# Kernel tuning notes

Measured on AMD Instinct MI355X. Metric: run time of the kernel, lower is better.

## Reference

```python
import jax, jax.numpy as jnp
import numpy as np

QLEN, KLEN, RLEN, BSZ, NHEAD, DHEAD = 512, 512, 1024, 8, 16, 64
SCALE = 0.125  # 1/sqrt(d_head)


def rel_shift(x, klen):
    # x: [q, r, b, n] -> [q, klen, b, n] (XLNet relative shift)
    q, r, b, n = x.shape
    x = x.reshape(r, q, b, n)[1:]
    x = x.reshape(q, r - 1, b, n)[:, :klen]
    return x


def setup_inputs() -> dict:
    key = jax.random.key(0)
    ks = jax.random.split(key, 9)
    q_head = jax.random.normal(ks[0], (QLEN, BSZ, NHEAD, DHEAD), jnp.float32)
    k_head_h = jax.random.normal(ks[1], (KLEN, BSZ, NHEAD, DHEAD), jnp.float32)
    v_head_h = jax.random.normal(ks[2], (KLEN, BSZ, NHEAD, DHEAD), jnp.float32)
    k_head_r = jax.random.normal(ks[3], (RLEN, BSZ, NHEAD, DHEAD), jnp.float32)
    seg_embed = jax.random.normal(ks[4], (2, NHEAD, DHEAD), jnp.float32)
    seg_mat = jax.random.randint(ks[5], (QLEN, KLEN, BSZ), 0, 2).astype(bool)
    r_w_bias = jax.random.normal(ks[6], (NHEAD, DHEAD), jnp.float32) * 0.02
    r_r_bias = jax.random.normal(ks[7], (NHEAD, DHEAD), jnp.float32) * 0.02
    r_s_bias = jax.random.normal(ks[8], (NHEAD, DHEAD), jnp.float32) * 0.02
    # causal attention mask: 1.0 where key position j > query position i
    attn_mask = (jnp.arange(KLEN)[None, :] > jnp.arange(QLEN)[:, None]).astype(jnp.float32)
    attn_mask = attn_mask[:, :, None, None]  # [q, k, 1, 1]
    return {
        "q_head": q_head, "k_head_h": k_head_h, "v_head_h": v_head_h,
        "k_head_r": k_head_r, "seg_embed": seg_embed, "seg_mat": seg_mat,
        "r_w_bias": r_w_bias, "r_r_bias": r_r_bias, "r_s_bias": r_s_bias,
        "attn_mask": attn_mask,
    }


def reference(q_head, k_head_h, v_head_h, k_head_r, seg_embed, seg_mat,
              r_w_bias, r_r_bias, r_s_bias, attn_mask):
    klen = k_head_h.shape[0]
    # content-based score: [q, k, b, n]
    ac = jnp.einsum('ibnd,jbnd->ijbn', q_head + r_w_bias, k_head_h)
    # position-based score with relative shift
    bd = jnp.einsum('ibnd,jbnd->ijbn', q_head + r_r_bias, k_head_r)
    bd = rel_shift(bd, klen)
    # segment-based score: ef [q, 2, b, n] -> select per (q,k,b) via seg_mat
    ef = jnp.einsum('ibnd,snd->isbn', q_head + r_s_bias, seg_embed)
    ef = jnp.where(seg_mat[:, :, :, None], ef[:, 1:, :, :], ef[:, :1, :, :])
    attn_score = (ac + bd + ef) * SCALE
    attn_score = attn_score - 1e30 * attn_mask
    attn_prob = jax.nn.softmax(attn_score, axis=1)  # softmax over key dim j
    # dropout is identity in eval mode
    attn_vec = jnp.einsum('ijbn,jbnd->ibnd', attn_prob, v_head_h)
    return attn_vec
```

## Files before the change

kernel.cpp:

```cpp
#include <hip/hip_runtime.h>

#define QLEN 512
#define KLEN 512
#define RLEN 1024
#define BSZ 8
#define NHEAD 16
#define DHEAD 64
#define SROW 8192
#define SCALEF 0.125f

typedef __bf16 bf16x8 __attribute__((ext_vector_type(8)));
typedef __bf16 bf16x4 __attribute__((ext_vector_type(4)));
typedef float  f32x4  __attribute__((ext_vector_type(4)));

__device__ __forceinline__ f32x4 mfma_bf16(bf16x8 a, bf16x8 b, f32x4 c) {
    return __builtin_amdgcn_mfma_f32_16x16x32_bf16(a, b, c, 0, 0, 0);
}

__device__ __forceinline__ bf16x8 cvt_frag(f32x4 a, f32x4 b) {
    bf16x8 f;
    f[0] = (__bf16)a[0]; f[1] = (__bf16)a[1]; f[2] = (__bf16)a[2]; f[3] = (__bf16)a[3];
    f[4] = (__bf16)b[0]; f[5] = (__bf16)b[1]; f[6] = (__bf16)b[2]; f[7] = (__bf16)b[3];
    return f;
}


__global__ void __launch_bounds__(256)
cvt_kernel(const float* __restrict__ src, __bf16* __restrict__ dst, int n4) {
    int idx = blockIdx.x * blockDim.x + threadIdx.x;
    const int stride = gridDim.x * blockDim.x;
    for (; idx < n4; idx += stride) {
        f32x4 v = ((const f32x4*)src)[idx];
        bf16x4 o;
        o[0] = (__bf16)v[0]; o[1] = (__bf16)v[1]; o[2] = (__bf16)v[2]; o[3] = (__bf16)v[3];
        ((bf16x4*)dst)[idx] = o;
    }
}

__global__ void __launch_bounds__(256)
vtr_kernel(const float* __restrict__ vh, __bf16* __restrict__ vt) {
    const int blk = blockIdx.x;
    const int ch  = blk & 15;
    const int hn  = blk >> 4;
    const int d   = threadIdx.x & 63;
    const int w   = threadIdx.x >> 6;
    const float* base = vh + (size_t)hn * DHEAD + d;
    bf16x8 o;
#pragma unroll
    for (int e = 0; e < 8; ++e) {
        const int j = ch * 32 + 4 * w + (e & 3) + 16 * (e >> 2);
        o[e] = (__bf16)base[(size_t)j * SROW];
    }
    *(bf16x8*)(vt + ((size_t)hn * DHEAD + d) * KLEN + ch * 32 + 8 * w) = o;
}

__global__ void __launch_bounds__(256)
relattn_v2(const float* __restrict__ q,  const __bf16* __restrict__ khb,
           const __bf16* __restrict__ vt, const __bf16* __restrict__ krb,
           const float* __restrict__ se, const void* __restrict__ segm,
           const float* __restrict__ rw, const float* __restrict__ rr,
           const float* __restrict__ rs, float* __restrict__ out)
{
    const int tid  = threadIdx.x;
    const int wv   = tid >> 6;
    const int lane = tid & 63;
    const int g    = lane >> 4;
    const int c    = lane & 15;
    const int qt8  = blockIdx.x & 7;
    const int hn   = blockIdx.x >> 3;
    const int b    = hn >> 4;
    const int n    = hn & 15;
    const int itile = qt8 + 8 * wv;
    const int i0   = itile << 4;
    const int i    = i0 + c;
    const size_t hoff = (size_t)hn * DHEAD;

    const __bf16* khh = khb + hoff;
    const __bf16* krh = krb + hoff;
    const __bf16* vth = vt + hoff * KLEN;

    const unsigned int* segw = (const unsigned int*)segm;
    const unsigned char* segb = (const unsigned char*)segm;
    unsigned int sacc = 0;
#pragma unroll
    for (int t = 0; t < 32; ++t) sacc |= segw[t];
    const bool seg4B = (sacc <= 1u) || (sacc == 0x3F800000u);

    bf16x8 qw[2], qr_[2], qs_[2];
    {
        const float* qrow = q + (size_t)i * SROW + hoff;
        const float* rwn = rw + n * DHEAD;
        const float* rrn = rr + n * DHEAD;
        const float* rsn = rs + n * DHEAD;
#pragma unroll
        for (int ks = 0; ks < 2; ++ks) {
            const int d0 = 32 * ks + 8 * g;
            f32x4 a0 = *(const f32x4*)(qrow + d0);
            f32x4 a1 = *(const f32x4*)(qrow + d0 + 4);
            qw[ks]  = cvt_frag(a0 + *(const f32x4*)(rwn + d0), a1 + *(const f32x4*)(rwn + d0 + 4));
            qr_[ks] = cvt_frag(a0 + *(const f32x4*)(rrn + d0), a1 + *(const f32x4*)(rrn + d0 + 4));
            qs_[ks] = cvt_frag(a0 + *(const f32x4*)(rsn + d0), a1 + *(const f32x4*)(rsn + d0 + 4));
        }
    }

    float e0, e1;
    {
        f32x4 eacc = {0.f, 0.f, 0.f, 0.f};
#pragma unroll
        for (int ks = 0; ks < 2; ++ks) {
            bf16x8 sfrag;
            if (c < 2) {
                const float* sp = se + ((size_t)c * NHEAD + n) * DHEAD + 32 * ks + 8 * g;
                sfrag = cvt_frag(*(const f32x4*)sp, *(const f32x4*)(sp + 4));
            } else {
#pragma unroll
                for (int e = 0; e < 8; ++e) sfrag[e] = (__bf16)0.f;
            }
            eacc = mfma_bf16(sfrag, qs_[ks], eacc);
        }
        e0 = __shfl(eacc[0], c, 64);
        e1 = __shfl(eacc[1], c, 64);
    }

    auto window_sh = [&](int base, float* wsh) {
        const __bf16* krow = krh + (size_t)(base + c) * SROW;
        bf16x8 k0 = *(const bf16x8*)(krow + 8 * g);
        bf16x8 k1 = *(const bf16x8*)(krow + 32 + 8 * g);
        f32x4 w = {0.f, 0.f, 0.f, 0.f};
        w = mfma_bf16(k0, qr_[0], w);
        w = mfma_bf16(k1, qr_[1], w);
        const int c3 = c & 3;
        const float w0 = w[0], w1 = w[1], w2 = w[2], w3 = w[3];
        const float r0 = (c3 == 0) ? w0 : (c3 == 1) ? w3 : (c3 == 2) ? w2 : w1;
        const float r1 = (c3 == 0) ? w1 : (c3 == 1) ? w0 : (c3 == 2) ? w3 : w2;
        const float r2 = (c3 == 0) ? w2 : (c3 == 1) ? w1 : (c3 == 2) ? w0 : w3;
        const float r3 = (c3 == 0) ? w3 : (c3 == 1) ? w2 : (c3 == 2) ? w1 : w0;
#pragma unroll
        for (int t = 0; t < 4; ++t) {
            const float rv = (t == 0) ? r0 : (t == 1) ? r1 : (t == 2) ? r2 : r3;
            const int rm  = (4 * g + t - c) & 15;
            const int src = ((rm >> 2) << 4) | c;
            wsh[t] = __shfl(rv, src, 64);
        }
    };

    float pw[4];
    window_sh(512 - i0 - 16, pw);

    auto do_tile = [&](int j0, float* stt) {
        const __bf16* krow = khh + (size_t)(j0 + c) * SROW;
        bf16x8 k0 = *(const bf16x8*)(krow + 8 * g);
        bf16x8 k1 = *(const bf16x8*)(krow + 32 + 8 * g);
        f32x4 acc = {0.f, 0.f, 0.f, 0.f};
        acc = mfma_bf16(k0, qw[0], acc);
        acc = mfma_bf16(k1, qw[1], acc);
        float cw[4];
        window_sh(512 + j0 - i0, cw);

        int sgv[4];
        const size_t sbase = ((size_t)i * KLEN + j0 + 4 * g) * BSZ + b;
        if (seg4B) {
#pragma unroll
            for (int t = 0; t < 4; ++t) sgv[t] = (segw[sbase + (size_t)t * BSZ] != 0u);
        } else {
#pragma unroll
            for (int t = 0; t < 4; ++t) sgv[t] = segb[sbase + (size_t)t * BSZ];
        }

#pragma unroll
        for (int t = 0; t < 4; ++t) {
            const int jr = 4 * g + t;
            const int j  = j0 + jr;
            const float bd = (jr >= c) ? cw[t] : pw[t];
            const float ef = sgv[t] ? e1 : e0;
            const float sv = (acc[t] + bd + ef) * SCALEF;
            stt[t] = (j <= i) ? sv : -1e30f;
            pw[t] = cw[t];
        }
    };

    f32x4 o0 = {0,0,0,0}, o1 = {0,0,0,0}, o2 = {0,0,0,0}, o3 = {0,0,0,0};
    float m_run = -3.0e38f, l_run = 0.f;

    const int nch = (itile >> 1) + 1;
    for (int ch = 0; ch < nch; ++ch) {
        const int jb = ch << 5;
        float st[8];
        do_tile(jb, st);
        if (jb + 16 <= i0) {
            do_tile(jb + 16, st + 4);
        } else {
            st[4] = st[5] = st[6] = st[7] = -1e30f;
        }

        float tm = fmaxf(fmaxf(fmaxf(st[0], st[1]), fmaxf(st[2], st[3])),
                         fmaxf(fmaxf(st[4], st[5]), fmaxf(st[6], st[7])));
        tm = fmaxf(tm, __shfl_xor(tm, 16, 64));
        tm = fmaxf(tm, __shfl_xor(tm, 32, 64));
        const float mnew = fmaxf(m_run, tm);
        const float scl  = __expf(m_run - mnew);
        float p[8];
#pragma unroll
        for (int t = 0; t < 8; ++t) p[t] = __expf(st[t] - mnew);
        float ls = ((p[0] + p[1]) + (p[2] + p[3])) + ((p[4] + p[5]) + (p[6] + p[7]));
        ls += __shfl_xor(ls, 16, 64);
        ls += __shfl_xor(ls, 32, 64);
        l_run = l_run * scl + ls;
        m_run = mnew;
        o0 *= scl; o1 *= scl; o2 *= scl; o3 *= scl;

        bf16x8 pf;
#pragma unroll
        for (int e = 0; e < 8; ++e) pf[e] = (__bf16)p[e];

#pragma unroll
        for (int dt = 0; dt < 4; ++dt) {
            bf16x8 vf = *(const bf16x8*)(vth + (size_t)(dt * 16 + c) * KLEN + jb + 8 * g);
            f32x4& od = (dt == 0) ? o0 : (dt == 1) ? o1 : (dt == 2) ? o2 : o3;
            od = mfma_bf16(vf, pf, od);
        }
    }

    const float inv = 1.f / l_run;
    float* orow = out + (size_t)i * SROW + hoff;
#pragma unroll
    for (int t = 0; t < 4; ++t) {
        orow[ 0 + 4 * g + t] = o0[t] * inv;
        orow[16 + 4 * g + t] = o1[t] * inv;
        orow[32 + 4 * g + t] = o2[t] * inv;
        orow[48 + 4 * g + t] = o3[t] * inv;
    }
}

__global__ void __launch_bounds__(256)
relattn_v1(const float* __restrict__ q,  const float* __restrict__ kh,
           const float* __restrict__ vh, const float* __restrict__ kr,
           const float* __restrict__ se, const void* __restrict__ segm,
           const float* __restrict__ rw, const float* __restrict__ rr,
           const float* __restrict__ rs, float* __restrict__ out)
{
    const int tid  = threadIdx.x;
    const int wv   = tid >> 6;
    const int lane = tid & 63;
    const int g    = lane >> 4;
    const int c    = lane & 15;
    const int qt8  = blockIdx.x & 7;
    const int hn   = blockIdx.x >> 3;
    const int b    = hn >> 4;
    const int n    = hn & 15;
    const int itile = qt8 + 8 * wv;
    const int i0   = itile << 4;
    const int i    = i0 + c;
    const size_t hoff = (size_t)hn * DHEAD;

    const float* khh = kh + hoff;
    const float* krh = kr + hoff;
    const float* vhh = vh + hoff;

    const unsigned int* segw = (const unsigned int*)segm;
    const unsigned char* segb = (const unsigned char*)segm;
    unsigned int sacc = 0;
#pragma unroll
    for (int t = 0; t < 32; ++t) sacc |= segw[t];
    const bool seg4B = (sacc <= 1u) || (sacc == 0x3F800000u);

    bf16x8 qw[2], qr_[2], qs_[2];
    {
        const float* qrow = q + (size_t)i * SROW + hoff;
        const float* rwn = rw + n * DHEAD;
        const float* rrn = rr + n * DHEAD;
        const float* rsn = rs + n * DHEAD;
#pragma unroll
        for (int ks = 0; ks < 2; ++ks) {
            const int d0 = 32 * ks + 4 * g;
            f32x4 a0 = *(const f32x4*)(qrow + d0);
            f32x4 a1 = *(const f32x4*)(qrow + d0 + 16);
            qw[ks]  = cvt_frag(a0 + *(const f32x4*)(rwn + d0), a1 + *(const f32x4*)(rwn + d0 + 16));
            qr_[ks] = cvt_frag(a0 + *(const f32x4*)(rrn + d0), a1 + *(const f32x4*)(rrn + d0 + 16));
            qs_[ks] = cvt_frag(a0 + *(const f32x4*)(rsn + d0), a1 + *(const f32x4*)(rsn + d0 + 16));
        }
    }

    float e0, e1;
    {
        f32x4 eacc = {0.f, 0.f, 0.f, 0.f};
#pragma unroll
        for (int ks = 0; ks < 2; ++ks) {
            bf16x8 sfrag;
            if (c < 2) {
                const float* sp = se + ((size_t)c * NHEAD + n) * DHEAD + 32 * ks + 4 * g;
                sfrag = cvt_frag(*(const f32x4*)sp, *(const f32x4*)(sp + 16));
            } else {
#pragma unroll
                for (int e = 0; e < 8; ++e) sfrag[e] = (__bf16)0.f;
            }
            eacc = mfma_bf16(sfrag, qs_[ks], eacc);
        }
        e0 = __shfl(eacc[0], c, 64);
        e1 = __shfl(eacc[1], c, 64);
    }

    auto window_sh = [&](int base, float* wsh) {
        const float* krow = krh + (size_t)(base + c) * SROW;
        bf16x8 k0 = cvt_frag(*(const f32x4*)(krow + 4 * g), *(const f32x4*)(krow + 4 * g + 16));
        bf16x8 k1 = cvt_frag(*(const f32x4*)(krow + 32 + 4 * g), *(const f32x4*)(krow + 48 + 4 * g));
        f32x4 w = {0.f, 0.f, 0.f, 0.f};
        w = mfma_bf16(k0, qr_[0], w);
        w = mfma_bf16(k1, qr_[1], w);
        const int c3 = c & 3;
        const float w0 = w[0], w1 = w[1], w2 = w[2], w3 = w[3];
        const float r0 = (c3 == 0) ? w0 : (c3 == 1) ? w3 : (c3 == 2) ? w2 : w1;
        const float r1 = (c3 == 0) ? w1 : (c3 == 1) ? w0 : (c3 == 2) ? w3 : w2;
        const float r2 = (c3 == 0) ? w2 : (c3 == 1) ? w1 : (c3 == 2) ? w0 : w3;
        const float r3 = (c3 == 0) ? w3 : (c3 == 1) ? w2 : (c3 == 2) ? w1 : w0;
#pragma unroll
        for (int t = 0; t < 4; ++t) {
            const float rv = (t == 0) ? r0 : (t == 1) ? r1 : (t == 2) ? r2 : r3;
            const int rm  = (4 * g + t - c) & 15;
            const int src = ((rm >> 2) << 4) | c;
            wsh[t] = __shfl(rv, src, 64);
        }
    };

    float pw[4];
    window_sh(512 - i0 - 16, pw);

    auto do_tile = [&](int j0, float* stt) {
        const float* krow = khh + (size_t)(j0 + c) * SROW;
        bf16x8 k0 = cvt_frag(*(const f32x4*)(krow + 4 * g), *(const f32x4*)(krow + 4 * g + 16));
        bf16x8 k1 = cvt_frag(*(const f32x4*)(krow + 32 + 4 * g), *(const f32x4*)(krow + 48 + 4 * g));
        f32x4 acc = {0.f, 0.f, 0.f, 0.f};
        acc = mfma_bf16(k0, qw[0], acc);
        acc = mfma_bf16(k1, qw[1], acc);
        float cw[4];
        window_sh(512 + j0 - i0, cw);

        int sgv[4];
        const size_t sbase = ((size_t)i * KLEN + j0 + 4 * g) * BSZ + b;
        if (seg4B) {
#pragma unroll
            for (int t = 0; t < 4; ++t) sgv[t] = (segw[sbase + (size_t)t * BSZ] != 0u);
        } else {
#pragma unroll
            for (int t = 0; t < 4; ++t) sgv[t] = segb[sbase + (size_t)t * BSZ];
        }

#pragma unroll
        for (int t = 0; t < 4; ++t) {
            const int jr = 4 * g + t;
            const int j  = j0 + jr;
            const float bd = (jr >= c) ? cw[t] : pw[t];
            const float ef = sgv[t] ? e1 : e0;
            const float sv = (acc[t] + bd + ef) * SCALEF;
            stt[t] = (j <= i) ? sv : -1e30f;
            pw[t] = cw[t];
        }
    };

    f32x4 o0 = {0,0,0,0}, o1 = {0,0,0,0}, o2 = {0,0,0,0}, o3 = {0,0,0,0};
    float m_run = -3.0e38f, l_run = 0.f;

    const int nch = (itile >> 1) + 1;
    for (int ch = 0; ch < nch; ++ch) {
        const int jb = ch << 5;
        float st[8];
        do_tile(jb, st);
        if (jb + 16 <= i0) {
            do_tile(jb + 16, st + 4);
        } else {
            st[4] = st[5] = st[6] = st[7] = -1e30f;
        }

        float tm = fmaxf(fmaxf(fmaxf(st[0], st[1]), fmaxf(st[2], st[3])),
                         fmaxf(fmaxf(st[4], st[5]), fmaxf(st[6], st[7])));
        tm = fmaxf(tm, __shfl_xor(tm, 16, 64));
        tm = fmaxf(tm, __shfl_xor(tm, 32, 64));
        const float mnew = fmaxf(m_run, tm);
        const float scl  = __expf(m_run - mnew);
        float p[8];
#pragma unroll
        for (int t = 0; t < 8; ++t) p[t] = __expf(st[t] - mnew);
        float ls = ((p[0] + p[1]) + (p[2] + p[3])) + ((p[4] + p[5]) + (p[6] + p[7]));
        ls += __shfl_xor(ls, 16, 64);
        ls += __shfl_xor(ls, 32, 64);
        l_run = l_run * scl + ls;
        m_run = mnew;
        o0 *= scl; o1 *= scl; o2 *= scl; o3 *= scl;

        bf16x8 pf;
#pragma unroll
        for (int e = 0; e < 8; ++e) pf[e] = (__bf16)p[e];

#pragma unroll
        for (int dt = 0; dt < 4; ++dt) {
            bf16x8 vf;
#pragma unroll
            for (int e = 0; e < 8; ++e) {
                const int j = jb + 4 * g + (e & 3) + ((e >> 2) << 4);
                const float vv = (j < KLEN) ? vhh[(size_t)j * SROW + dt * 16 + c] : 0.f;
                vf[e] = (__bf16)vv;
            }
            f32x4& od = (dt == 0) ? o0 : (dt == 1) ? o1 : (dt == 2) ? o2 : o3;
            od = mfma_bf16(vf, pf, od);
        }
    }

    const float inv = 1.f / l_run;
    float* orow = out + (size_t)i * SROW + hoff;
#pragma unroll
    for (int t = 0; t < 4; ++t) {
        orow[ 0 + 4 * g + t] = o0[t] * inv;
        orow[16 + 4 * g + t] = o1[t] * inv;
        orow[32 + 4 * g + t] = o2[t] * inv;
        orow[48 + 4 * g + t] = o3[t] * inv;
    }
}

extern "C" void kernel_launch(void* const* d_in, const int* in_sizes, int n_in,
                              void* d_out, int out_size, void* d_ws, size_t ws_size,
                              hipStream_t stream) {
    const float* q  = (const float*)d_in[0];
    const float* kh = (const float*)d_in[1];
    const float* vh = (const float*)d_in[2];
    const float* kr = (const float*)d_in[3];
    const float* se = (const float*)d_in[4];
    const void*  sm = (const void*)d_in[5];
    const float* rw = (const float*)d_in[6];
    const float* rr = (const float*)d_in[7];
    const float* rs = (const float*)d_in[8];
    float* out = (float*)d_out;
    (void)in_sizes; (void)n_in; (void)out_size;

    const size_t vt_e = (size_t)BSZ * NHEAD * DHEAD * KLEN;
    const size_t kh_e = (size_t)KLEN * SROW;
    const size_t kr_e = (size_t)RLEN * SROW;
    const size_t need = (vt_e + kh_e + kr_e) * sizeof(__bf16);

    if (ws_size >= need) {
        __bf16* wsb = (__bf16*)d_ws;
        __bf16* vt  = wsb;
        __bf16* khb = wsb + vt_e;
        __bf16* krb = wsb + vt_e + kh_e;
        cvt_kernel<<<dim3(1024), dim3(256), 0, stream>>>(kh, khb, (int)(kh_e / 4));
        cvt_kernel<<<dim3(1024), dim3(256), 0, stream>>>(kr, krb, (int)(kr_e / 4));
        vtr_kernel<<<dim3(2048), dim3(256), 0, stream>>>(vh, vt);
        relattn_v2<<<dim3(1024), dim3(256), 0, stream>>>(q, khb, vt, krb, se, sm, rw, rr, rs, out);
    } else {
        relattn_v1<<<dim3(1024), dim3(256), 0, stream>>>(q, kh, vh, kr, se, sm, rw, rr, rs, out);
    }
}
```

Measured before the change: 242.5 us.

## Pack segment mask to bits, balance causal tiles per wave, prefetch chunk operands

Adds a segpack kernel that turns the strided per-element segment mask into one 32-bit word per (batch, 32-key chunk, query), so the attention kernel reads a single word instead of scattered bytes or words. The attention kernel now runs 128-thread blocks, and each wave handles a pair of query tiles (itile and 31-itile) to even out causal work across waves. Key and relative-key fragments for the next chunk are loaded into a second register set while the current chunk is computed. This costs an extra kernel launch, more registers per thread and fewer resident waves per block, in exchange for less latency stalling and better load balance.

Result: faster. 231.9 us (-4.4%).

```diff
diff --git a/kernel.cpp b/kernel.cpp
--- a/kernel.cpp
+++ b/kernel.cpp
@@ -55,9 +55,42 @@
 }
 
 __global__ void __launch_bounds__(256)
-relattn_v2(const float* __restrict__ q,  const __bf16* __restrict__ khb,
+segpack_kernel(const void* __restrict__ segm, unsigned int* __restrict__ packed) {
+    const int i   = blockIdx.x;
+    const int tid = threadIdx.x;
+    __shared__ unsigned int lds[4096];
+    const unsigned int* segw = (const unsigned int*)segm;
+    const unsigned char* segb = (const unsigned char*)segm;
+    unsigned int sacc = 0;
+#pragma unroll
+    for (int t = 0; t < 32; ++t) sacc |= segw[t];
+    const bool seg4B = (sacc <= 1u) || (sacc == 0x3F800000u);
+    if (seg4B) {
+        for (int t = tid; t < 4096; t += 256) lds[t] = segw[(size_t)i * 4096 + t];
+    } else {
+        for (int t = tid; t < 4096; t += 256) lds[t] = segb[(size_t)i * 4096 + t];
+    }
+    __syncthreads();
+    if (tid < 128) {
+        const int b = tid & 7, jw = tid >> 3;
+        unsigned int word = 0;
+#pragma unroll
+        for (int jj = 0; jj < 32; ++jj)
+            if (lds[(jw * 32 + jj) * 8 + b]) word |= (1u << jj);
+        packed[((size_t)b * 16 + jw) * 512 + i] = word;
+    }
+}
+
+struct ChunkRegs {
+    bf16x8 kh0a, kh1a, kh0b, kh1b;
+    bf16x8 kr0a, kr1a, kr0b, kr1b;
+    unsigned int sw;
+};
+
+__global__ void __launch_bounds__(128)
+relattn_v3(const float* __restrict__ q,  const __bf16* __restrict__ khb,
            const __bf16* __restrict__ vt, const __bf16* __restrict__ krb,
-           const float* __restrict__ se, const void* __restrict__ segm,
+           const float* __restrict__ se, const unsigned int* __restrict__ segpk,
            const float* __restrict__ rw, const float* __restrict__ rr,
            const float* __restrict__ rs, float* __restrict__ out)
 {
@@ -66,169 +99,196 @@
     const int lane = tid & 63;
     const int g    = lane >> 4;
     const int c    = lane & 15;
-    const int qt8  = blockIdx.x & 7;
+    const int pairi = ((blockIdx.x & 7) << 1) | wv;
     const int hn   = blockIdx.x >> 3;
     const int b    = hn >> 4;
     const int n    = hn & 15;
-    const int itile = qt8 + 8 * wv;
-    const int i0   = itile << 4;
-    const int i    = i0 + c;
     const size_t hoff = (size_t)hn * DHEAD;
 
     const __bf16* khh = khb + hoff;
     const __bf16* krh = krb + hoff;
     const __bf16* vth = vt + hoff * KLEN;
-
-    const unsigned int* segw = (const unsigned int*)segm;
-    const unsigned char* segb = (const unsigned char*)segm;
-    unsigned int sacc = 0;
-#pragma unroll
-    for (int t = 0; t < 32; ++t) sacc |= segw[t];
-    const bool seg4B = (sacc <= 1u) || (sacc == 0x3F800000u);
-
-    bf16x8 qw[2], qr_[2], qs_[2];
-    {
-        const float* qrow = q + (size_t)i * SROW + hoff;
-        const float* rwn = rw + n * DHEAD;
-        const float* rrn = rr + n * DHEAD;
-        const float* rsn = rs + n * DHEAD;
-#pragma unroll
-        for (int ks = 0; ks < 2; ++ks) {
-            const int d0 = 32 * ks + 8 * g;
-            f32x4 a0 = *(const f32x4*)(qrow + d0);
-            f32x4 a1 = *(const f32x4*)(qrow + d0 + 4);
-            qw[ks]  = cvt_frag(a0 + *(const f32x4*)(rwn + d0), a1 + *(const f32x4*)(rwn + d0 + 4));
-            qr_[ks] = cvt_frag(a0 + *(const f32x4*)(rrn + d0), a1 + *(const f32x4*)(rrn + d0 + 4));
-            qs_[ks] = cvt_frag(a0 + *(const f32x4*)(rsn + d0), a1 + *(const f32x4*)(rsn + d0 + 4));
-        }
-    }
-
-    float e0, e1;
-    {
-        f32x4 eacc = {0.f, 0.f, 0.f, 0.f};
-#pragma unroll
-        for (int ks = 0; ks < 2; ++ks) {
-            bf16x8 sfrag;
-            if (c < 2) {
-                const float* sp = se + ((size_t)c * NHEAD + n) * DHEAD + 32 * ks + 8 * g;
-                sfrag = cvt_frag(*(const f32x4*)sp, *(const f32x4*)(sp + 4));
+    const unsigned int* spb = segpk + (size_t)b * 16 * 512;
+    const float* rwn = rw + n * DHEAD;
+    const float* rrn = rr + n * DHEAD;
+    const float* rsn = rs + n * DHEAD;
+
+#pragma unroll 1
+    for (int half = 0; half < 2; ++half) {
+        const int itile = half ? (31 - pairi) : pairi;
+        const int i0 = itile << 4;
+        const int i  = i0 + c;
+
+        bf16x8 qw[2], qr_[2], qs_[2];
+        {
+            const float* qrow = q + (size_t)i * SROW + hoff;
+#pragma unroll
+            for (int ks = 0; ks < 2; ++ks) {
+                const int d0 = 32 * ks + 8 * g;
+                f32x4 a0 = *(const f32x4*)(qrow + d0);
+                f32x4 a1 = *(const f32x4*)(qrow + d0 + 4);
+                qw[ks]  = cvt_frag(a0 + *(const f32x4*)(rwn + d0), a1 + *(const f32x4*)(rwn + d0 + 4));
+                qr_[ks] = cvt_frag(a0 + *(const f32x4*)(rrn + d0), a1 + *(const f32x4*)(rrn + d0 + 4));
+                qs_[ks] = cvt_frag(a0 + *(const f32x4*)(rsn + d0), a1 + *(const f32x4*)(rsn + d0 + 4));
+            }
+        }
+
+        float e0, e1;
+        {
+            f32x4 eacc = {0.f, 0.f, 0.f, 0.f};
+#pragma unroll
+            for (int ks = 0; ks < 2; ++ks) {
+                bf16x8 sfrag;
+                if (c < 2) {
+                    const float* sp = se + ((size_t)c * NHEAD + n) * DHEAD + 32 * ks + 8 * g;
+                    sfrag = cvt_frag(*(const f32x4*)sp, *(const f32x4*)(sp + 4));
+                } else {
+#pragma unroll
+                    for (int e = 0; e < 8; ++e) sfrag[e] = (__bf16)0.f;
+                }
+                eacc = mfma_bf16(sfrag, qs_[ks], eacc);
+            }
+            e0 = __shfl(eacc[0], c, 64);
+            e1 = __shfl(eacc[1], c, 64);
+        }
+
+        auto windowc = [&](bf16x8 k0, bf16x8 k1, float* wsh) {
+            f32x4 w = {0.f, 0.f, 0.f, 0.f};
+            w = mfma_bf16(k0, qr_[0], w);
+            w = mfma_bf16(k1, qr_[1], w);
+            const int c3 = c & 3;
+            const float w0 = w[0], w1 = w[1], w2 = w[2], w3 = w[3];
+            const float r0 = (c3 == 0) ? w0 : (c3 == 1) ? w3 : (c3 == 2) ? w2 : w1;
+            const float r1 = (c3 == 0) ? w1 : (c3 == 1) ? w0 : (c3 == 2) ? w3 : w2;
+            const float r2 = (c3 == 0) ? w2 : (c3 == 1) ? w1 : (c3 == 2) ? w0 : w3;
+            const float r3 = (c3 == 0) ? w3 : (c3 == 1) ? w2 : (c3 == 2) ? w1 : w0;
+#pragma unroll
+            for (int t = 0; t < 4; ++t) {
+                const float rv = (t == 0) ? r0 : (t == 1) ? r1 : (t == 2) ? r2 : r3;
+                const int rm  = (4 * g + t - c) & 15;
+                const int src = ((rm >> 2) << 4) | c;
+                wsh[t] = __shfl(rv, src, 64);
+            }
+        };
+
+        float pw[4];
+        {
+            const __bf16* krow = krh + (size_t)(512 - i0 - 16 + c) * SROW;
+            windowc(*(const bf16x8*)(krow + 8 * g), *(const bf16x8*)(krow + 32 + 8 * g), pw);
+        }
+
+        const int nch = (itile >> 1) + 1;
+
+        auto LOADC = [&](int ch, ChunkRegs& R) {
+            const int jb = ch << 5;
+            const int r2 = jb + 16 + c;
+            const __bf16* p1 = khh + (size_t)(jb + c) * SROW;
+            R.kh0a = *(const bf16x8*)(p1 + 8 * g);
+            R.kh1a = *(const bf16x8*)(p1 + 32 + 8 * g);
+            const __bf16* p2 = khh + (size_t)(r2 < KLEN ? r2 : KLEN - 1) * SROW;
+            R.kh0b = *(const bf16x8*)(p2 + 8 * g);
+            R.kh1b = *(const bf16x8*)(p2 + 32 + 8 * g);
+            const int wb1 = 512 + jb - i0 + c;
+            const __bf16* p3 = krh + (size_t)wb1 * SROW;
+            R.kr0a = *(const bf16x8*)(p3 + 8 * g);
+            R.kr1a = *(const bf16x8*)(p3 + 32 + 8 * g);
+            const __bf16* p4 = krh + (size_t)(wb1 + 16) * SROW;
+            R.kr0b = *(const bf16x8*)(p4 + 8 * g);
+            R.kr1b = *(const bf16x8*)(p4 + 32 + 8 * g);
+            R.sw = spb[(size_t)(jb >> 5) * 512 + i];
+        };
+
+        f32x4 o0 = {0,0,0,0}, o1 = {0,0,0,0}, o2 = {0,0,0,0}, o3 = {0,0,0,0};
+        float m_run = -3.0e38f, l_run = 0.f;
+
+        auto COMPUTE = [&](int ch, ChunkRegs& R) {
+            const int jb = ch << 5;
+            float st[8];
+            {
+                f32x4 acc = {0.f, 0.f, 0.f, 0.f};
+                acc = mfma_bf16(R.kh0a, qw[0], acc);
+                acc = mfma_bf16(R.kh1a, qw[1], acc);
+                float cw[4];
+                windowc(R.kr0a, R.kr1a, cw);
+#pragma unroll
+                for (int t = 0; t < 4; ++t) {
+                    const int jr = 4 * g + t;
+                    const int j  = jb + jr;
+                    const float bd = (jr >= c) ? cw[t] : pw[t];
+                    const float ef = ((R.sw >> (4 * g + t)) & 1u) ? e1 : e0;
+                    const float sv = (acc[t] + bd + ef) * SCALEF;
+                    st[t] = (j <= i) ? sv : -1e30f;
+                    pw[t] = cw[t];
+                }
+            }
+            if (jb + 16 <= i0) {
+                f32x4 acc = {0.f, 0.f, 0.f, 0.f};
+                acc = mfma_bf16(R.kh0b, qw[0], acc);
+                acc = mfma_bf16(R.kh1b, qw[1], acc);
+                float cw[4];
+                windowc(R.kr0b, R.kr1b, cw);
+#pragma unroll
+                for (int t = 0; t < 4; ++t) {
+                    const int jr = 4 * g + t;
+                    const int j  = jb + 16 + jr;
+                    const float bd = (jr >= c) ? cw[t] : pw[t];
+                    const float ef = ((R.sw >> (16 + 4 * g + t)) & 1u) ? e1 : e0;
+                    const float sv = (acc[t] + bd + ef) * SCALEF;
+                    st[4 + t] = (j <= i) ? sv : -1e30f;
+                    pw[t] = cw[t];
+                }
             } else {
-#pragma unroll
-                for (int e = 0; e < 8; ++e) sfrag[e] = (__bf16)0.f;
-            }
-            eacc = mfma_bf16(sfrag, qs_[ks], eacc);
-        }
-        e0 = __shfl(eacc[0], c, 64);
-        e1 = __shfl(eacc[1], c, 64);
-    }
-
-    auto window_sh = [&](int base, float* wsh) {
-        const __bf16* krow = krh + (size_t)(base + c) * SROW;
-        bf16x8 k0 = *(const bf16x8*)(krow + 8 * g);
-        bf16x8 k1 = *(const bf16x8*)(krow + 32 + 8 * g);
-        f32x4 w = {0.f, 0.f, 0.f, 0.f};
-        w = mfma_bf16(k0, qr_[0], w);
-        w = mfma_bf16(k1, qr_[1], w);
-        const int c3 = c & 3;
-        const float w0 = w[0], w1 = w[1], w2 = w[2], w3 = w[3];
-        const float r0 = (c3 == 0) ? w0 : (c3 == 1) ? w3 : (c3 == 2) ? w2 : w1;
-        const float r1 = (c3 == 0) ? w1 : (c3 == 1) ? w0 : (c3 == 2) ? w3 : w2;
-        const float r2 = (c3 == 0) ? w2 : (c3 == 1) ? w1 : (c3 == 2) ? w0 : w3;
-        const float r3 = (c3 == 0) ? w3 : (c3 == 1) ? w2 : (c3 == 2) ? w1 : w0;
+                st[4] = st[5] = st[6] = st[7] = -1e30f;
+            }
+
+            float tm = fmaxf(fmaxf(fmaxf(st[0], st[1]), fmaxf(st[2], st[3])),
+                             fmaxf(fmaxf(st[4], st[5]), fmaxf(st[6], st[7])));
+            tm = fmaxf(tm, __shfl_xor(tm, 16, 64));
+            tm = fmaxf(tm, __shfl_xor(tm, 32, 64));
+            const float mnew = fmaxf(m_run, tm);
+            const float scl  = __expf(m_run - mnew);
+            float p[8];
+#pragma unroll
+            for (int t = 0; t < 8; ++t) p[t] = __expf(st[t] - mnew);
+            float ls = ((p[0] + p[1]) + (p[2] + p[3])) + ((p[4] + p[5]) + (p[6] + p[7]));
+            ls += __shfl_xor(ls, 16, 64);
+            ls += __shfl_xor(ls, 32, 64);
+            l_run = l_run * scl + ls;
+            m_run = mnew;
+            o0 *= scl; o1 *= scl; o2 *= scl; o3 *= scl;
+
+            bf16x8 pf;
+#pragma unroll
+            for (int e = 0; e < 8; ++e) pf[e] = (__bf16)p[e];
+#pragma unroll
+            for (int dt = 0; dt < 4; ++dt) {
+                bf16x8 vf = *(const bf16x8*)(vth + (size_t)(dt * 16 + c) * KLEN + jb + 8 * g);
+                f32x4& od = (dt == 0) ? o0 : (dt == 1) ? o1 : (dt == 2) ? o2 : o3;
+                od = mfma_bf16(vf, pf, od);
+            }
+        };
+
+        ChunkRegs A, B;
+        LOADC(0, A);
+        int ch = 0;
+        while (true) {
+            if (ch + 1 < nch) LOADC(ch + 1, B);
+            COMPUTE(ch, A);
+            if (++ch >= nch) break;
+            if (ch + 1 < nch) LOADC(ch + 1, A);
+            COMPUTE(ch, B);
+            if (++ch >= nch) break;
+        }
+
+        const float inv = 1.f / l_run;
+        float* orow = out + (size_t)i * SROW + hoff;
 #pragma unroll
         for (int t = 0; t < 4; ++t) {
-            const float rv = (t == 0) ? r0 : (t == 1) ? r1 : (t == 2) ? r2 : r3;
-            const int rm  = (4 * g + t - c) & 15;
-            const int src = ((rm >> 2) << 4) | c;
-            wsh[t] = __shfl(rv, src, 64);
-        }
-    };
-
-    float pw[4];
-    window_sh(512 - i0 - 16, pw);
-
-    auto do_tile = [&](int j0, float* stt) {
-        const __bf16* krow = khh + (size_t)(j0 + c) * SROW;
-        bf16x8 k0 = *(const bf16x8*)(krow + 8 * g);
-        bf16x8 k1 = *(const bf16x8*)(krow + 32 + 8 * g);
-        f32x4 acc = {0.f, 0.f, 0.f, 0.f};
-        acc = mfma_bf16(k0, qw[0], acc);
-        acc = mfma_bf16(k1, qw[1], acc);
-        float cw[4];
-        window_sh(512 + j0 - i0, cw);
-
-        int sgv[4];
-        const size_t sbase = ((size_t)i * KLEN + j0 + 4 * g) * BSZ + b;
-        if (seg4B) {
-#pragma unroll
-            for (int t = 0; t < 4; ++t) sgv[t] = (segw[sbase + (size_t)t * BSZ] != 0u);
-        } else {
-#pragma unroll
-            for (int t = 0; t < 4; ++t) sgv[t] = segb[sbase + (size_t)t * BSZ];
-        }
-
-#pragma unroll
-        for (int t = 0; t < 4; ++t) {
-            const int jr = 4 * g + t;
-            const int j  = j0 + jr;
-            const float bd = (jr >= c) ? cw[t] : pw[t];
-            const float ef = sgv[t] ? e1 : e0;
-            const float sv = (acc[t] + bd + ef) * SCALEF;
-            stt[t] = (j <= i) ? sv : -1e30f;
-            pw[t] = cw[t];
-        }
-    };
-
-    f32x4 o0 = {0,0,0,0}, o1 = {0,0,0,0}, o2 = {0,0,0,0}, o3 = {0,0,0,0};
-    float m_run = -3.0e38f, l_run = 0.f;
-
-    const int nch = (itile >> 1) + 1;
-    for (int ch = 0; ch < nch; ++ch) {
-        const int jb = ch << 5;
-        float st[8];
-        do_tile(jb, st);
-        if (jb + 16 <= i0) {
-            do_tile(jb + 16, st + 4);
-        } else {
-            st[4] = st[5] = st[6] = st[7] = -1e30f;
-        }
-
-        float tm = fmaxf(fmaxf(fmaxf(st[0], st[1]), fmaxf(st[2], st[3])),
-                         fmaxf(fmaxf(st[4], st[5]), fmaxf(st[6], st[7])));
-        tm = fmaxf(tm, __shfl_xor(tm, 16, 64));
-        tm = fmaxf(tm, __shfl_xor(tm, 32, 64));
-        const float mnew = fmaxf(m_run, tm);
-        const float scl  = __expf(m_run - mnew);
-        float p[8];
-#pragma unroll
-        for (int t = 0; t < 8; ++t) p[t] = __expf(st[t] - mnew);
-        float ls = ((p[0] + p[1]) + (p[2] + p[3])) + ((p[4] + p[5]) + (p[6] + p[7]));
-        ls += __shfl_xor(ls, 16, 64);
-        ls += __shfl_xor(ls, 32, 64);
-        l_run = l_run * scl + ls;
-        m_run = mnew;
-        o0 *= scl; o1 *= scl; o2 *= scl; o3 *= scl;
-
-        bf16x8 pf;
-#pragma unroll
-        for (int e = 0; e < 8; ++e) pf[e] = (__bf16)p[e];
-
-#pragma unroll
-        for (int dt = 0; dt < 4; ++dt) {
-            bf16x8 vf = *(const bf16x8*)(vth + (size_t)(dt * 16 + c) * KLEN + jb + 8 * g);
-            f32x4& od = (dt == 0) ? o0 : (dt == 1) ? o1 : (dt == 2) ? o2 : o3;
-            od = mfma_bf16(vf, pf, od);
-        }
-    }
-
-    const float inv = 1.f / l_run;
-    float* orow = out + (size_t)i * SROW + hoff;
-#pragma unroll
-    for (int t = 0; t < 4; ++t) {
-        orow[ 0 + 4 * g + t] = o0[t] * inv;
-        orow[16 + 4 * g + t] = o1[t] * inv;
-        orow[32 + 4 * g + t] = o2[t] * inv;
-        orow[48 + 4 * g + t] = o3[t] * inv;
+            orow[ 0 + 4 * g + t] = o0[t] * inv;
+            orow[16 + 4 * g + t] = o1[t] * inv;
+            orow[32 + 4 * g + t] = o2[t] * inv;
+            orow[48 + 4 * g + t] = o3[t] * inv;
+        }
     }
 }
 
@@ -434,17 +494,20 @@
     const size_t vt_e = (size_t)BSZ * NHEAD * DHEAD * KLEN;
     const size_t kh_e = (size_t)KLEN * SROW;
     const size_t kr_e = (size_t)RLEN * SROW;
-    const size_t need = (vt_e + kh_e + kr_e) * sizeof(__bf16);
+    const size_t sp_w = (size_t)BSZ * 16 * 512;
+    const size_t need = (vt_e + kh_e + kr_e) * sizeof(__bf16) + sp_w * 4;
 
     if (ws_size >= need) {
         __bf16* wsb = (__bf16*)d_ws;
         __bf16* vt  = wsb;
         __bf16* khb = wsb + vt_e;
         __bf16* krb = wsb + vt_e + kh_e;
+        unsigned int* segpk = (unsigned int*)(wsb + vt_e + kh_e + kr_e);
         cvt_kernel<<<dim3(1024), dim3(256), 0, stream>>>(kh, khb, (int)(kh_e / 4));
         cvt_kernel<<<dim3(1024), dim3(256), 0, stream>>>(kr, krb, (int)(kr_e / 4));
         vtr_kernel<<<dim3(2048), dim3(256), 0, stream>>>(vh, vt);
-        relattn_v2<<<dim3(1024), dim3(256), 0, stream>>>(q, khb, vt, krb, se, sm, rw, rr, rs, out);
+        segpack_kernel<<<dim3(512), dim3(256), 0, stream>>>(sm, segpk);
+        relattn_v3<<<dim3(1024), dim3(128), 0, stream>>>(q, khb, vt, krb, se, segpk, rw, rr, rs, out);
     } else {
         relattn_v1<<<dim3(1024), dim3(256), 0, stream>>>(q, kh, vh, kr, se, sm, rw, rr, rs, out);
     }
```
